# Performance work log

Measured on AMD Instinct MI355X. Metric: run time of the kernel, lower is better.

Reference implementation:

```python
import jax, jax.numpy as jnp
import numpy as np

IMSIZE = 128; R = 2; B = 2; C = 3; D = 64; Q = 128; M = 8; ITERS = 32
N = IMSIZE * IMSIZE
EPS = 1e-8


def _build_edges(S, r):
    # local (2r+1)^2 pixel neighborhood, as in build_perception(imsize, perception_size)
    ys, xs = np.meshgrid(np.arange(S), np.arange(S), indexing='ij')
    rows, cols = [], []
    for dy in range(-r, r + 1):
        for dx in range(-r, r + 1):
            ny, nx = ys + dy, xs + dx
            ok = (ny >= 0) & (ny < S) & (nx >= 0) & (nx < S)
            rows.append((ys * S + xs)[ok])
            cols.append((ny * S + nx)[ok])
    return (np.concatenate(rows).astype(np.int32), np.concatenate(cols).astype(np.int32))


def _conv(x, w, b=None):
    y = jax.lax.conv_general_dilated(x, w, (1, 1), 'SAME', dimension_numbers=('NHWC', 'HWIO', 'NHWC'))
    return y if b is None else y + b


def _bn(x, g, b):
    mu = x.mean((0, 1, 2))
    var = x.var((0, 1, 2))
    return (x - mu) * jax.lax.rsqrt(var + 1e-5) * g + b


def _resblock(f, w1, g1, t1, w2, g2, t2):
    h = jax.nn.relu(_bn(_conv(f, w1), g1, t1))
    h = _bn(_conv(h, w2), g2, t2)
    return jax.nn.relu(f + h)


def _forward(x, w_bb1, b_bb1, w_bb2, b_bb2,
             w_k1, g_k1, t_k1, w_k2, g_k2, t_k2, w_kp, b_kp,
             w_q1, g_q1, t_q1, w_q2, g_q2, t_q2, w_qp,
             h0, row, col, agent_idx):
    # conv backbone (preserves spatial resolution)
    f = jax.nn.relu(_conv(x, w_bb1, b_bb1))
    f = jax.nn.relu(_conv(f, w_bb2, b_bb2))
    # key / query heads: ResidualBlock + 1x1 conv
    ks = _conv(_resblock(f, w_k1, g_k1, t_k1, w_k2, g_k2, t_k2), w_kp, b_kp).reshape(B, N, D)
    qs = _conv(_resblock(f, w_q1, g_q1, t_q1, w_q2, g_q2, t_q2), w_qp).reshape(B, N, D)
    # edge-gather cosine similarity (torch.cosine_similarity with eps=1e-8)
    qe = qs[:, row]          # [B, E, D]
    ke = ks[:, col]          # [B, E, D]
    weights = (qe * ke).sum(-1) / (
        jnp.maximum(jnp.linalg.norm(qe, axis=-1), EPS) *
        jnp.maximum(jnp.linalg.norm(ke, axis=-1), EPS))   # [B, E]

    # 32-iteration sparse adjacency propagation: h <- normalize(A @ h)
    def step(h, _):
        msg = jnp.zeros_like(h).at[:, row, :].add(weights[:, :, None] * h[:, col, :])
        h = msg / jnp.maximum(jnp.linalg.norm(msg, axis=-1, keepdims=True), EPS)
        return h, None

    h, _ = jax.lax.scan(step, h0, None, length=ITERS)     # [B, N, Q]

    # competition routing: pixels compete for M agent slots via cosine affinity
    pix = h / jnp.maximum(jnp.linalg.norm(h, axis=-1, keepdims=True), EPS)
    ag = pix[:, agent_idx]                                # [B, M, Q]
    sim = jnp.einsum('bnq,bmq->bnm', pix, ag)
    masks = jax.nn.softmax(sim * 10.0, axis=-1)           # [B, N, M]
    return masks.reshape(B, IMSIZE, IMSIZE, M).transpose(0, 3, 1, 2)  # [B, M, W, H]


def setup_inputs() -> dict:
    key = jax.random.key(0)
    k = jax.random.split(key, 12)
    s = 0.05
    row, col = _build_edges(IMSIZE, R)
    agent_idx = np.linspace(0, N - 1, M).astype(np.int32)
    return dict(
        x=jax.random.normal(k[0], (B, IMSIZE, IMSIZE, C), jnp.float32),
        w_bb1=jax.random.normal(k[1], (3, 3, C, D), jnp.float32) * s, b_bb1=jnp.zeros((D,), jnp.float32),
        w_bb2=jax.random.normal(k[2], (3, 3, D, D), jnp.float32) * s, b_bb2=jnp.zeros((D,), jnp.float32),
        w_k1=jax.random.normal(k[3], (3, 3, D, D), jnp.float32) * s,
        g_k1=jnp.ones((D,), jnp.float32), t_k1=jnp.zeros((D,), jnp.float32),
        w_k2=jax.random.normal(k[4], (3, 3, D, D), jnp.float32) * s,
        g_k2=jnp.ones((D,), jnp.float32), t_k2=jnp.zeros((D,), jnp.float32),
        w_kp=jax.random.normal(k[5], (1, 1, D, D), jnp.float32) * s, b_kp=jnp.zeros((D,), jnp.float32),
        w_q1=jax.random.normal(k[6], (3, 3, D, D), jnp.float32) * s,
        g_q1=jnp.ones((D,), jnp.float32), t_q1=jnp.zeros((D,), jnp.float32),
        w_q2=jax.random.normal(k[7], (3, 3, D, D), jnp.float32) * s,
        g_q2=jnp.ones((D,), jnp.float32), t_q2=jnp.zeros((D,), jnp.float32),
        w_qp=jax.random.normal(k[8], (1, 1, D, D), jnp.float32) * s,
        h0=jax.random.normal(k[9], (B, N, Q), jnp.float32),
        row=jnp.asarray(row), col=jnp.asarray(col),
        agent_idx=jnp.asarray(agent_idx),
    )


def reference(x, w_bb1, b_bb1, w_bb2, b_bb2,
              w_k1, g_k1, t_k1, w_k2, g_k2, t_k2, w_kp, b_kp,
              w_q1, g_q1, t_q1, w_q2, g_q2, t_q2, w_qp,
              h0, row, col, agent_idx):
    return _forward(x, w_bb1, b_bb1, w_bb2, b_bb2,
                    w_k1, g_k1, t_k1, w_k2, g_k2, t_k2, w_kp, b_kp,
                    w_q1, g_q1, t_q1, w_q2, g_q2, t_q2, w_qp,
                    h0, row, col, agent_idx)
```

## Files before the change

### kernel.cpp

```cpp
#include <hip/hip_runtime.h>
#include <math.h>

#define NPIX 16384
#define EPSF 1e-8f

typedef float f32x4 __attribute__((ext_vector_type(4)));
typedef short s16x8 __attribute__((ext_vector_type(8)));

__device__ __forceinline__ float wred64(float s){
  s += __shfl_xor(s, 32); s += __shfl_xor(s, 16); s += __shfl_xor(s, 8);
  s += __shfl_xor(s, 4);  s += __shfl_xor(s, 2);  s += __shfl_xor(s, 1);
  return s;
}
__device__ __forceinline__ float rdlane(float v, int l){
  return __int_as_float(__builtin_amdgcn_readlane(__float_as_int(v), l));
}
__device__ __forceinline__ float dot4f(float4 a, float4 b, float acc){
  acc = fmaf(a.x,b.x,acc); acc = fmaf(a.y,b.y,acc);
  acc = fmaf(a.z,b.z,acc); acc = fmaf(a.w,b.w,acc);
  return acc;
}
__device__ __forceinline__ void bf16split(float v, unsigned short &hi, unsigned short &lo){
  unsigned u = __float_as_uint(v);
  unsigned r = u + 0x7FFFu + ((u >> 16) & 1u);
  hi = (unsigned short)(r >> 16);
  float hf = __uint_as_float(((unsigned)hi) << 16);
  float l = v - hf;
  unsigned u2 = __float_as_uint(l);
  unsigned r2 = u2 + 0x7FFFu + ((u2 >> 16) & 1u);
  lo = (unsigned short)(r2 >> 16);
}

__global__ __launch_bounds__(256) void prep_kernel(const float* __restrict__ w_bb2, const float* __restrict__ w_k1,
                            const float* __restrict__ w_k2, const float* __restrict__ w_q1,
                            const float* __restrict__ w_q2, const float* __restrict__ w_kp,
                            const float* __restrict__ w_qp, unsigned short* __restrict__ wh,
                            unsigned short* __restrict__ wl, float* __restrict__ wtp,
                            float* __restrict__ stats){
  int gid = blockIdx.x*256 + threadIdx.x;
  if (gid < 184320){
    int j = gid & 7;
    int t1 = gid >> 3;
    int lane = t1 & 63;
    int t2 = t1 >> 6;
    int kb = t2 % 18;
    int t3 = t2 / 18;
    int ct = t3 & 3;
    int c  = t3 >> 2;
    const float* src = c==0? w_bb2 : c==1? w_k1 : c==2? w_k2 : c==3? w_q1 : w_q2;
    int cout = ct*16 + (lane & 15);
    int k = kb*32 + (lane>>4)*8 + j;
    float v = src[k*64 + cout];
    unsigned short h,l; bf16split(v,h,l);
    wh[gid] = h; wl[gid] = l;
  } else if (gid < 192512){
    int t = gid - 184320; int which = t >> 12; int d = t & 4095;
    const float* src = which ? w_qp : w_kp;
    int k = d & 3, cout = (d>>2) & 63, cin4 = d >> 8;
    wtp[t] = src[(cin4*4 + k)*64 + cout];
  } else if (gid < 193024){
    stats[gid - 192512] = 0.f;
  }
}

__global__ __launch_bounds__(256) void conv1_kernel(const float* __restrict__ x, const float* __restrict__ w,
                                                    const float* __restrict__ bias, float* __restrict__ out){
  int wv = blockIdx.x*4 + (threadIdx.x >> 6);
  int c  = threadIdx.x & 63;
  int p0 = wv << 3;
  int ub = __builtin_amdgcn_readfirstlane(p0);
  int b  = ub >> 14; int i0 = ub & (NPIX-1);
  int y  = i0 >> 7, x0 = i0 & 127;
  float wv_[9][3];
  #pragma unroll
  for (int t=0;t<9;++t)
    #pragma unroll
    for (int ci=0;ci<3;++ci) wv_[t][ci] = w[(t*3+ci)*64 + c];
  float bv = bias[c];
  float acc[8];
  #pragma unroll
  for (int p=0;p<8;++p) acc[p] = bv;
  for (int ky=0; ky<3; ++ky){
    int ny = y + ky - 1;
    if ((unsigned)ny >= 128u) continue;
    const float* rowp = x + ((b<<14) + ny*128)*3;
    for (int kx=0; kx<3; ++kx){
      int t = ky*3 + kx;
      #pragma unroll
      for (int p=0;p<8;++p){
        int col = x0 + p + kx - 1;
        if ((unsigned)col < 128u){
          const float* ip = rowp + col*3;
          acc[p] = fmaf(ip[0], wv_[t][0], acc[p]);
          acc[p] = fmaf(ip[1], wv_[t][1], acc[p]);
          acc[p] = fmaf(ip[2], wv_[t][2], acc[p]);
        }
      }
    }
  }
  float* op = out + (p0 << 6) + c;
  #pragma unroll
  for (int p=0;p<8;++p) op[p*64] = fmaxf(acc[p], 0.f);
}

__global__ __launch_bounds__(512) void conv3m_kernel(const float* __restrict__ in,
    const unsigned short* __restrict__ wh, const unsigned short* __restrict__ wl,
    const float* __restrict__ bias, int relu,
    const float* __restrict__ bnst, const float* __restrict__ bng, const float* __restrict__ bnb,
    float* __restrict__ out, float* __restrict__ ost){
  __shared__ char smem[50688];
  unsigned short* lhi = (unsigned short*)smem;
  float* lout = (float*)smem;
  __shared__ float la[64], lb[64];
  __shared__ float ls1[64], ls2[64];
  int blk = blockIdx.x;
  int xh = blk & 1, y = (blk>>1) & 127, b = blk >> 8;
  int x0 = xh << 6;
  int tid = threadIdx.x;
  if (tid < 64){
    float a = 1.f, bo = 0.f;
    if (bnst){
      float mu  = bnst[tid] * (1.f/32768.f);
      float var = bnst[64+tid] * (1.f/32768.f) - mu*mu;
      a  = bng[tid] * rsqrtf(var + 1e-5f);
      bo = bnb[tid] - mu*a;
    }
    la[tid] = a; lb[tid] = bo;
    ls1[tid] = 0.f; ls2[tid] = 0.f;
  }
  __syncthreads();
  for (int s = tid; s < 3168; s += 512){
    int pr = s >> 4, cq = s & 15;
    int ky = pr / 66, px = pr - ky*66;
    int ny = y + ky - 1, gx = x0 - 1 + px;
    float v0=0.f, v1=0.f, v2=0.f, v3=0.f;
    if ((unsigned)ny < 128u && (unsigned)gx < 128u){
      const float* ip = in + (((b<<14) + ny*128 + gx)<<6) + (cq<<2);
      float4 t = *(const float4*)ip;
      int c0 = cq<<2;
      v0 = fmaxf(fmaf(t.x, la[c0],   lb[c0]),   0.f);
      v1 = fmaxf(fmaf(t.y, la[c0+1], lb[c0+1]), 0.f);
      v2 = fmaxf(fmaf(t.z, la[c0+2], lb[c0+2]), 0.f);
      v3 = fmaxf(fmaf(t.w, la[c0+3], lb[c0+3]), 0.f);
    }
    unsigned short h0,l0,h1,l1,h2,l2,h3,l3;
    bf16split(v0,h0,l0); bf16split(v1,h1,l1); bf16split(v2,h2,l2); bf16split(v3,h3,l3);
    int slot = (cq >> 1) ^ (pr & 7);
    int byte = pr*128 + (slot<<4) + ((cq & 1) << 3);
    *(uint2*)(smem + byte) = make_uint2((unsigned)h0 | ((unsigned)h1<<16),
                                        (unsigned)h2 | ((unsigned)h3<<16));
    *(uint2*)(smem + 25344 + byte) = make_uint2((unsigned)l0 | ((unsigned)l1<<16),
                                                (unsigned)l2 | ((unsigned)l3<<16));
  }
  __syncthreads();
  int lane = tid & 63, wid = tid >> 6;
  int pxsub = wid & 3, ch = wid >> 2;
  int col16 = lane & 15, kgrp = lane >> 4;
  f32x4 acc0 = {0.f,0.f,0.f,0.f}, acc1 = acc0, acl0 = acc0, acl1 = acc0;
  int abase = (ch*2*18)*512 + lane*8;
  #pragma unroll
  for (int kb=0; kb<18; ++kb){
    int tap = kb >> 1;
    int ky = (tap >= 6) ? 2 : (tap >= 3 ? 1 : 0);
    int kx = tap - ky*3;
    int pr = ky*66 + pxsub*16 + col16 + kx;
    int ci0 = ((kb & 1) << 5) + (kgrp << 3);
    int byte = pr*128 + ((((ci0 >> 3) ^ (pr & 7))) << 4);
    s16x8 Bh = *(const s16x8*)(smem + byte);
    s16x8 Bl = *(const s16x8*)(smem + 25344 + byte);
    int ao = abase + kb*512;
    s16x8 Ah0 = *(const s16x8*)(wh + ao);
    s16x8 Al0 = *(const s16x8*)(wl + ao);
    s16x8 Ah1 = *(const s16x8*)(wh + ao + 9216);
    s16x8 Al1 = *(const s16x8*)(wl + ao + 9216);
    acc0 = __builtin_amdgcn_mfma_f32_16x16x32_bf16(Ah0, Bh, acc0, 0, 0, 0);
    acl0 = __builtin_amdgcn_mfma_f32_16x16x32_bf16(Ah0, Bl, acl0, 0, 0, 0);
    acc1 = __builtin_amdgcn_mfma_f32_16x16x32_bf16(Ah1, Bh, acc1, 0, 0, 0);
    acl1 = __builtin_amdgcn_mfma_f32_16x16x32_bf16(Ah1, Bl, acl1, 0, 0, 0);
    acl0 = __builtin_amdgcn_mfma_f32_16x16x32_bf16(Al0, Bh, acl0, 0, 0, 0);
    acl1 = __builtin_amdgcn_mfma_f32_16x16x32_bf16(Al1, Bh, acl1, 0, 0, 0);
  }
  acc0 = acc0 + acl0;
  acc1 = acc1 + acl1;
  __syncthreads();
  int pxl = pxsub*16 + col16;
  int co0 = ch*32 + kgrp*4;
  *(f32x4*)(lout + pxl*68 + co0)      = acc0;
  *(f32x4*)(lout + pxl*68 + co0 + 16) = acc1;
  __syncthreads();
  {
    int px = tid >> 3, c8 = (tid & 7) << 3;
    const float* lp = lout + px*68 + c8;
    float r0[8];
    #pragma unroll
    for (int j=0;j<8;++j) r0[j] = lp[j];
    if (bias){
      #pragma unroll
      for (int j=0;j<8;++j) r0[j] += bias[c8+j];
    }
    if (relu){
      #pragma unroll
      for (int j=0;j<8;++j) r0[j] = fmaxf(r0[j], 0.f);
    }
    float* op = out + (((b<<14) + y*128 + x0 + px)<<6) + c8;
    #pragma unroll
    for (int j=0;j<8;++j) op[j] = r0[j];
    if (ost){
      float s1v[8], s2v[8];
      #pragma unroll
      for (int j=0;j<8;++j){ s1v[j] = r0[j]; s2v[j] = r0[j]*r0[j]; }
      #pragma unroll
      for (int m=8; m<64; m<<=1){
        #pragma unroll
        for (int j=0;j<8;++j){ s1v[j] += __shfl_xor(s1v[j], m); s2v[j] += __shfl_xor(s2v[j], m); }
      }
      int lane2 = tid & 63;
      if ((lane2 >> 3) == 0){
        int c0 = (lane2 & 7) << 3;
        #pragma unroll
        for (int j=0;j<8;++j){ atomicAdd(&ls1[c0+j], s1v[j]); atomicAdd(&ls2[c0+j], s2v[j]); }
      }
      __syncthreads();
      if (tid < 64){ atomicAdd(&ost[tid], ls1[tid]); atomicAdd(&ost[64+tid], ls2[tid]); }
    }
  }
}

__global__ __launch_bounds__(512) void conv3m2_kernel(const float* __restrict__ in,
    const unsigned short* __restrict__ whA, const unsigned short* __restrict__ wlA,
    const unsigned short* __restrict__ whB, const unsigned short* __restrict__ wlB,
    float* __restrict__ outA, float* __restrict__ ostA,
    float* __restrict__ outB, float* __restrict__ ostB){
  __shared__ char smem[50688];
  float* loutA = (float*)smem;
  float* loutB = (float*)smem + 4352;
  __shared__ float ls1A[64], ls2A[64], ls1B[64], ls2B[64];
  int blk = blockIdx.x;
  int xh = blk & 1, y = (blk>>1) & 127, b = blk >> 8;
  int x0 = xh << 6;
  int tid = threadIdx.x;
  if (tid < 64){ ls1A[tid]=0.f; ls2A[tid]=0.f; ls1B[tid]=0.f; ls2B[tid]=0.f; }
  __syncthreads();
  for (int s = tid; s < 3168; s += 512){
    int pr = s >> 4, cq = s & 15;
    int ky = pr / 66, px = pr - ky*66;
    int ny = y + ky - 1, gx = x0 - 1 + px;
    float v0=0.f, v1=0.f, v2=0.f, v3=0.f;
    if ((unsigned)ny < 128u && (unsigned)gx < 128u){
      const float* ip = in + (((b<<14) + ny*128 + gx)<<6) + (cq<<2);
      float4 t = *(const float4*)ip;
      v0 = t.x; v1 = t.y; v2 = t.z; v3 = t.w;
    }
    unsigned short h0,l0,h1,l1,h2,l2,h3,l3;
    bf16split(v0,h0,l0); bf16split(v1,h1,l1); bf16split(v2,h2,l2); bf16split(v3,h3,l3);
    int slot = (cq >> 1) ^ (pr & 7);
    int byte = pr*128 + (slot<<4) + ((cq & 1) << 3);
    *(uint2*)(smem + byte) = make_uint2((unsigned)h0 | ((unsigned)h1<<16),
                                        (unsigned)h2 | ((unsigned)h3<<16));
    *(uint2*)(smem + 25344 + byte) = make_uint2((unsigned)l0 | ((unsigned)l1<<16),
                                                (unsigned)l2 | ((unsigned)l3<<16));
  }
  __syncthreads();
  int lane = tid & 63, wid = tid >> 6;
  int pxsub = wid & 3, ch = wid >> 2;
  int col16 = lane & 15, kgrp = lane >> 4;
  f32x4 z = {0.f,0.f,0.f,0.f};
  f32x4 aA0=z, aA1=z, lA0=z, lA1=z, aB0=z, aB1=z, lB0=z, lB1=z;
  int abase = (ch*2*18)*512 + lane*8;
  #pragma unroll
  for (int kb=0; kb<18; ++kb){
    int tap = kb >> 1;
    int ky = (tap >= 6) ? 2 : (tap >= 3 ? 1 : 0);
    int kx = tap - ky*3;
    int pr = ky*66 + pxsub*16 + col16 + kx;
    int ci0 = ((kb & 1) << 5) + (kgrp << 3);
    int byte = pr*128 + ((((ci0 >> 3) ^ (pr & 7))) << 4);
    s16x8 Bh = *(const s16x8*)(smem + byte);
    s16x8 Bl = *(const s16x8*)(smem + 25344 + byte);
    int ao = abase + kb*512;
    s16x8 AhA0 = *(const s16x8*)(whA + ao);
    s16x8 AlA0 = *(const s16x8*)(wlA + ao);
    s16x8 AhA1 = *(const s16x8*)(whA + ao + 9216);
    s16x8 AlA1 = *(const s16x8*)(wlA + ao + 9216);
    s16x8 AhB0 = *(const s16x8*)(whB + ao);
    s16x8 AlB0 = *(const s16x8*)(wlB + ao);
    s16x8 AhB1 = *(const s16x8*)(whB + ao + 9216);
    s16x8 AlB1 = *(const s16x8*)(wlB + ao + 9216);
    aA0 = __builtin_amdgcn_mfma_f32_16x16x32_bf16(AhA0, Bh, aA0, 0, 0, 0);
    lA0 = __builtin_amdgcn_mfma_f32_16x16x32_bf16(AhA0, Bl, lA0, 0, 0, 0);
    aA1 = __builtin_amdgcn_mfma_f32_16x16x32_bf16(AhA1, Bh, aA1, 0, 0, 0);
    lA1 = __builtin_amdgcn_mfma_f32_16x16x32_bf16(AhA1, Bl, lA1, 0, 0, 0);
    lA0 = __builtin_amdgcn_mfma_f32_16x16x32_bf16(AlA0, Bh, lA0, 0, 0, 0);
    lA1 = __builtin_amdgcn_mfma_f32_16x16x32_bf16(AlA1, Bh, lA1, 0, 0, 0);
    aB0 = __builtin_amdgcn_mfma_f32_16x16x32_bf16(AhB0, Bh, aB0, 0, 0, 0);
    lB0 = __builtin_amdgcn_mfma_f32_16x16x32_bf16(AhB0, Bl, lB0, 0, 0, 0);
    aB1 = __builtin_amdgcn_mfma_f32_16x16x32_bf16(AhB1, Bh, aB1, 0, 0, 0);
    lB1 = __builtin_amdgcn_mfma_f32_16x16x32_bf16(AhB1, Bl, lB1, 0, 0, 0);
    lB0 = __builtin_amdgcn_mfma_f32_16x16x32_bf16(AlB0, Bh, lB0, 0, 0, 0);
    lB1 = __builtin_amdgcn_mfma_f32_16x16x32_bf16(AlB1, Bh, lB1, 0, 0, 0);
  }
  aA0 = aA0 + lA0; aA1 = aA1 + lA1;
  aB0 = aB0 + lB0; aB1 = aB1 + lB1;
  __syncthreads();
  int pxl = pxsub*16 + col16;
  int co0 = ch*32 + kgrp*4;
  *(f32x4*)(loutA + pxl*68 + co0)      = aA0;
  *(f32x4*)(loutA + pxl*68 + co0 + 16) = aA1;
  *(f32x4*)(loutB + pxl*68 + co0)      = aB0;
  *(f32x4*)(loutB + pxl*68 + co0 + 16) = aB1;
  __syncthreads();
  {
    int px = tid >> 3, c8 = (tid & 7) << 3;
    int lane2 = tid & 63;
    float rA[8], rB[8];
    #pragma unroll
    for (int j=0;j<8;++j){ rA[j] = loutA[px*68 + c8 + j]; rB[j] = loutB[px*68 + c8 + j]; }
    float* opA = outA + (((b<<14) + y*128 + x0 + px)<<6) + c8;
    float* opB = outB + (((b<<14) + y*128 + x0 + px)<<6) + c8;
    #pragma unroll
    for (int j=0;j<8;++j){ opA[j] = rA[j]; opB[j] = rB[j]; }
    float sA1[8], sA2[8], sB1[8], sB2[8];
    #pragma unroll
    for (int j=0;j<8;++j){ sA1[j]=rA[j]; sA2[j]=rA[j]*rA[j]; sB1[j]=rB[j]; sB2[j]=rB[j]*rB[j]; }
    #pragma unroll
    for (int m=8; m<64; m<<=1){
      #pragma unroll
      for (int j=0;j<8;++j){
        sA1[j] += __shfl_xor(sA1[j], m); sA2[j] += __shfl_xor(sA2[j], m);
        sB1[j] += __shfl_xor(sB1[j], m); sB2[j] += __shfl_xor(sB2[j], m);
      }
    }
    if ((lane2 >> 3) == 0){
      int c0 = (lane2 & 7) << 3;
      #pragma unroll
      for (int j=0;j<8;++j){
        atomicAdd(&ls1A[c0+j], sA1[j]); atomicAdd(&ls2A[c0+j], sA2[j]);
        atomicAdd(&ls1B[c0+j], sB1[j]); atomicAdd(&ls2B[c0+j], sB2[j]);
      }
    }
    __syncthreads();
    if (tid < 64){
      atomicAdd(&ostA[tid], ls1A[tid]); atomicAdd(&ostA[64+tid], ls2A[tid]);
      atomicAdd(&ostB[tid], ls1B[tid]); atomicAdd(&ostB[64+tid], ls2B[tid]);
    }
  }
}

__global__ __launch_bounds__(256) void resfuse2_kernel(float* __restrict__ tk, float* __restrict__ tq,
                                                       const float* __restrict__ f, const float* __restrict__ ST,
                                                       const float* __restrict__ gk, const float* __restrict__ bk,
                                                       const float* __restrict__ gq, const float* __restrict__ bq){
  int gid = blockIdx.x*256 + threadIdx.x;
  int isQ = gid >> 19;
  int idx4 = gid & 524287;
  float* t = isQ ? tq : tk;
  const float* stats = ST + (isQ ? 384 : 128);
  const float* g    = isQ ? gq : gk;
  const float* beta = isQ ? bq : bk;
  float4 v = ((float4*)t)[idx4];
  float4 fv = ((const float4*)f)[idx4];
  int c0 = (idx4 & 15) * 4;
  float a[4], bb[4];
  #pragma unroll
  for (int j=0;j<4;++j){
    int c = c0 + j;
    float mu  = stats[c]    * (1.f/32768.f);
    float var = stats[64+c] * (1.f/32768.f) - mu*mu;
    a[j]  = g[c] * rsqrtf(var + 1e-5f);
    bb[j] = beta[c] - mu*a[j];
  }
  v.x = fmaxf(fv.x + fmaf(v.x, a[0], bb[0]), 0.f);
  v.y = fmaxf(fv.y + fmaf(v.y, a[1], bb[1]), 0.f);
  v.z = fmaxf(fv.z + fmaf(v.z, a[2], bb[2]), 0.f);
  v.w = fmaxf(fv.w + fmaf(v.w, a[3], bb[3]), 0.f);
  ((float4*)t)[idx4] = v;
}

__global__ __launch_bounds__(256) void proj2_kernel(const float* __restrict__ rk, const float* __restrict__ rq,
                                                    const float* __restrict__ wtp, const float* __restrict__ bkp,
                                                    float* __restrict__ outk, float* __restrict__ outq,
                                                    float* __restrict__ nk, float* __restrict__ nq){
  int wvg = blockIdx.x*4 + (threadIdx.x >> 6);
  int isQ = wvg >> 12;
  int wv = wvg & 4095;
  int c  = threadIdx.x & 63;
  const float* r = isQ ? rq : rk;
  const float* wt1 = wtp + (isQ ? 4096 : 0);
  float* out = isQ ? outq : outk;
  float* nrm = isQ ? nq : nk;
  int p0 = wv << 3;
  int ub = __builtin_amdgcn_readfirstlane(p0);
  const float4* wq = (const float4*)wt1 + c;
  float4 w[16];
  #pragma unroll
  for (int q=0;q<16;++q) w[q] = wq[q*64];
  float bv = isQ ? 0.f : bkp[c];
  #pragma unroll
  for (int p=0;p<8;++p){
    const float* ip = r + ((ub + p) << 6);
    float a0 = bv, a1 = 0.f;
    #pragma unroll
    for (int q=0;q<16;q+=2){
      float4 i0 = *(const float4*)(ip + (q<<2));
      float4 i1 = *(const float4*)(ip + ((q+1)<<2));
      a0 = dot4f(i0, w[q],   a0);
      a1 = dot4f(i1, w[q+1], a1);
    }
    float acc = a0 + a1;
    out[((p0+p)<<6) + c] = acc;
    float s = wred64(acc*acc);
    if (c == 0) nrm[p0+p] = sqrtf(s);
  }
}

#define EW_PAD 68
__global__ __launch_bounds__(256) void edge_kernel(const float* __restrict__ qs, const float* __restrict__ ks,
                                                   const float* __restrict__ nq, const float* __restrict__ nk,
                                                   float* __restrict__ W){
  __shared__ float klds[100*EW_PAD];
  __shared__ float qlds[16*EW_PAD];
  int blk = blockIdx.x;
  int b = blk >> 10; int rem = blk & 1023;
  int y = rem >> 3; int x0 = (rem & 7) << 4;
  int tid = threadIdx.x;
  for (int s = tid; s < 1600; s += 256){
    int cin4 = s & 15; int col = (s >> 4) % 20; int r = (s >> 4) / 20;
    int ry = y - 2 + r; ry = ry < 0 ? 0 : (ry > 127 ? 127 : ry);
    int cx = x0 - 2 + col; cx = cx < 0 ? 0 : (cx > 127 ? 127 : cx);
    float4 v = *(const float4*)(ks + (((b<<14) + ry*128 + cx)<<6) + cin4*4);
    *(float4*)(klds + (r*20+col)*EW_PAD + cin4*4) = v;
  }
  {
    int cin4 = tid & 15; int px = tid >> 4;
    float4 v = *(const float4*)(qs + (((b<<14) + y*128 + x0 + px)<<6) + cin4*4);
    *(float4*)(qlds + px*EW_PAD + cin4*4) = v;
  }
  __syncthreads();
  #pragma unroll
  for (int pair=0; pair<2; ++pair){
    int t2 = tid + pair*256;
    int px = t2 >> 5; int o = t2 & 31;
    if (o < 25){
      int dy = o/5 - 2, dx = o%5 - 2;
      int yy = y + dy, xx = x0 + px + dx;
      bool valid = ((unsigned)yy < 128u) && ((unsigned)xx < 128u);
      const float* kq = klds + ((dy+2)*20 + (px+dx+2))*EW_PAD;
      const float* qq = qlds + px*EW_PAD;
      float a0 = 0.f, a1 = 0.f;
      #pragma unroll
      for (int q=0; q<16; q+=2){
        a0 = dot4f(*(const float4*)(qq + q*4),     *(const float4*)(kq + q*4),     a0);
        a1 = dot4f(*(const float4*)(qq + (q+1)*4), *(const float4*)(kq + (q+1)*4), a1);
      }
      float acc = a0 + a1;
      int gp = (b<<14) + y*128 + x0 + px;
      float wv_ = 0.f;
      if (valid){
        int gj = (b<<14) + yy*128 + xx;
        float rq = 1.f / fmaxf(nq[gp], EPSF);
        float rk = 1.f / fmaxf(nk[gj], EPSF);
        wv_ = acc * rq * rk;
      }
      W[gp*25 + o] = wv_;
    }
  }
}

__global__ __launch_bounds__(256) void mp_iter_kernel(const float* __restrict__ src, float* __restrict__ dst,
                                                      const float* __restrict__ W){
  int lane = threadIdx.x & 63;
  int wid  = threadIdx.x >> 6;
  int blk  = blockIdx.x;
  int xcd = blk & 7, s = blk >> 3;
  int row_id = xcd*32 + (s >> 3);
  int q8 = s & 7;
  int b = row_id >> 7, y = row_id & 127;
  int x0 = ((q8 << 2) + wid) << 2;
  int gp0 = (b << 14) + y*128 + x0;
  int lo = lane < 25 ? lane : 24;
  float wv[4];
  #pragma unroll
  for (int p=0;p<4;++p) wv[p] = W[(gp0+p)*25 + lo];
  const float* rp[5];
  #pragma unroll
  for (int r=0;r<5;++r){
    int ry = y - 2 + r; ry = ry < 0 ? 0 : (ry > 127 ? 127 : ry);
    rp[r] = src + (((b<<14) + ry*128) << 7) + lane;
  }
  float wa[5][5], wb[5][5];
  #pragma unroll
  for (int cc=0; cc<4; ++cc){
    int xc = x0 - 2 + cc; if (xc < 0) xc = 0;
    int off = xc << 7;
    #pragma unroll
    for (int r=0;r<5;++r){ wa[r][cc] = rp[r][off]; wb[r][cc] = rp[r][off + 64]; }
  }
  #pragma unroll
  for (int p=0;p<4;++p){
    int xl = x0 + p + 2; if (xl > 127) xl = 127;
    int off = xl << 7;
    #pragma unroll
    for (int r=0;r<5;++r){ wa[r][4] = rp[r][off]; wb[r][4] = rp[r][off + 64]; }
    float a0 = 0.f, a1 = 0.f;
    #pragma unroll
    for (int r=0;r<5;++r){
      #pragma unroll
      for (int cc=0;cc<5;++cc){
        float w = rdlane(wv[p], r*5+cc);
        a0 = fmaf(w, wa[r][cc], a0);
        a1 = fmaf(w, wb[r][cc], a1);
      }
    }
    float ss = wred64(a0*a0 + a1*a1);
    float sc = 1.f / fmaxf(sqrtf(ss), EPSF);
    float* dp = dst + ((gp0 + p) << 7) + lane;
    dp[0] = a0*sc; dp[64] = a1*sc;
    #pragma unroll
    for (int r=0;r<5;++r){
      #pragma unroll
      for (int cc=0;cc<4;++cc){ wa[r][cc] = wa[r][cc+1]; wb[r][cc] = wb[r][cc+1]; }
    }
  }
}

__global__ __launch_bounds__(256) void mp_last_kernel(const float* __restrict__ src, const float* __restrict__ W,
                                                      const int* __restrict__ agidx, float* __restrict__ out){
  int lane = threadIdx.x & 63;
  int wid  = threadIdx.x >> 6;
  int blk  = blockIdx.x;
  int xcd = blk & 7, s = blk >> 3;
  int row_id = xcd*32 + (s >> 2);
  int q4 = s & 3;
  int b = row_id >> 7, y = row_id & 127;
  int x0 = ((q4 << 2) + wid) << 3;
  int gp0 = (b << 14) + y*128 + x0;
  int lo = lane < 25 ? lane : 24;
  float av0[8], av1[8], isc[8];
  #pragma unroll
  for (int m=0;m<8;++m){
    int ai = agidx[m];
    int ay = ai >> 7, ax = ai & 127;
    float wva = W[((b<<14) + ai)*25 + lo];
    float aa0 = 0.f, aa1 = 0.f;
    #pragma unroll
    for (int r=0;r<5;++r){
      int ry = ay - 2 + r; ry = ry < 0 ? 0 : (ry > 127 ? 127 : ry);
      const float* rp = src + (((b<<14) + ry*128) << 7) + lane;
      #pragma unroll
      for (int cc=0;cc<5;++cc){
        int xc = ax - 2 + cc; xc = xc < 0 ? 0 : (xc > 127 ? 127 : xc);
        float w = rdlane(wva, r*5+cc);
        aa0 = fmaf(w, rp[xc<<7], aa0);
        aa1 = fmaf(w, rp[(xc<<7) + 64], aa1);
      }
    }
    float ssm = wred64(aa0*aa0 + aa1*aa1);
    isc[m] = 1.f / fmaxf(sqrtf(ssm), EPSF);
    av0[m] = aa0; av1[m] = aa1;
  }
  float wv[8];
  #pragma unroll
  for (int p=0;p<8;++p) wv[p] = W[(gp0+p)*25 + lo];
  const float* rp[5];
  #pragma unroll
  for (int r=0;r<5;++r){
    int ry = y - 2 + r; ry = ry < 0 ? 0 : (ry > 127 ? 127 : ry);
    rp[r] = src + (((b<<14) + ry*128) << 7) + lane;
  }
  float wa[5][5], wb[5][5];
  #pragma unroll
  for (int cc=0; cc<4; ++cc){
    int xc = x0 - 2 + cc; if (xc < 0) xc = 0;
    int off = xc << 7;
    #pragma unroll
    for (int r=0;r<5;++r){ wa[r][cc] = rp[r][off]; wb[r][cc] = rp[r][off + 64]; }
  }
  #pragma unroll
  for (int p=0;p<8;++p){
    int xl = x0 + p + 2; if (xl > 127) xl = 127;
    int off = xl << 7;
    #pragma unroll
    for (int r=0;r<5;++r){ wa[r][4] = rp[r][off]; wb[r][4] = rp[r][off + 64]; }
    float a0 = 0.f, a1 = 0.f;
    #pragma unroll
    for (int r=0;r<5;++r){
      #pragma unroll
      for (int cc=0;cc<5;++cc){
        float w = rdlane(wv[p], r*5+cc);
        a0 = fmaf(w, wa[r][cc], a0);
        a1 = fmaf(w, wb[r][cc], a1);
      }
    }
    float ss = wred64(a0*a0 + a1*a1);
    float sc = 1.f / fmaxf(sqrtf(ss), EPSF);
    float p0 = a0*sc, p1 = a1*sc;
    float sim[8];
    #pragma unroll
    for (int m=0;m<8;++m)
      sim[m] = wred64(p0*av0[m] + p1*av1[m]) * isc[m];
    float mx = sim[0];
    #pragma unroll
    for (int m=1;m<8;++m) mx = fmaxf(mx, sim[m]);
    float e[8]; float sum = 0.f;
    #pragma unroll
    for (int m=0;m<8;++m){ e[m] = __expf((sim[m]-mx)*10.f); sum += e[m]; }
    float rs = 1.f / sum;
    if (lane < 8){
      float val = e[0];
      #pragma unroll
      for (int m=1;m<8;++m) val = (lane==m) ? e[m] : val;
      out[(((b<<3)+lane)<<14) + y*128 + x0 + p] = val * rs;
    }
    #pragma unroll
    for (int r=0;r<5;++r){
      #pragma unroll
      for (int cc=0;cc<4;++cc){ wa[r][cc] = wa[r][cc+1]; wb[r][cc] = wb[r][cc+1]; }
    }
  }
}

extern "C" void kernel_launch(void* const* d_in, const int* in_sizes, int n_in,
                              void* d_out, int out_size, void* d_ws, size_t ws_size,
                              hipStream_t stream) {
  (void)in_sizes; (void)n_in; (void)out_size; (void)ws_size;
  const float* x     = (const float*)d_in[0];
  const float* w_bb1 = (const float*)d_in[1];
  const float* b_bb1 = (const float*)d_in[2];
  const float* w_bb2 = (const float*)d_in[3];
  const float* b_bb2 = (const float*)d_in[4];
  const float* w_k1  = (const float*)d_in[5];
  const float* g_k1  = (const float*)d_in[6];
  const float* t_k1  = (const float*)d_in[7];
  const float* w_k2  = (const float*)d_in[8];
  const float* g_k2  = (const float*)d_in[9];
  const float* t_k2  = (const float*)d_in[10];
  const float* w_kp  = (const float*)d_in[11];
  const float* b_kp  = (const float*)d_in[12];
  const float* w_q1  = (const float*)d_in[13];
  const float* g_q1  = (const float*)d_in[14];
  const float* t_q1  = (const float*)d_in[15];
  const float* w_q2  = (const float*)d_in[16];
  const float* g_q2  = (const float*)d_in[17];
  const float* t_q2  = (const float*)d_in[18];
  const float* w_qp  = (const float*)d_in[19];
  const float* h0    = (const float*)d_in[20];
  const int*   agidx = (const int*)d_in[23];
  float* out = (float*)d_out;
  float* ws  = (float*)d_ws;

  float* S0 = ws + 0;
  float* S1 = ws + 2097152;
  float* S2 = ws + 4194304;
  float* S3 = ws + 6291456;
  float* S4 = ws + 8388608;
  float* WW = ws + 12582912;
  float* NK = ws + 13402112;
  float* NQ = ws + 13434880;
  float* ST = ws + 13467648;
  float* WTp = ws + 13470208;
  unsigned short* WH = (unsigned short*)(ws + 13478400);
  unsigned short* WL = WH + 184320;
  float* HA = ws + 0;
  float* HB = ws + 4194304;

  prep_kernel<<<754, 256, 0, stream>>>(w_bb2, w_k1, w_k2, w_q1, w_q2, w_kp, w_qp, WH, WL, WTp, ST);
  conv1_kernel<<<1024, 256, 0, stream>>>(x, w_bb1, b_bb1, S0);
  conv3m_kernel<<<512, 512, 0, stream>>>(S0, WH + 0, WL + 0, b_bb2, 1, nullptr, nullptr, nullptr, S1, nullptr);
  conv3m2_kernel<<<512, 512, 0, stream>>>(S1, WH + 36864, WL + 36864, WH + 3*36864, WL + 3*36864,
                                          S2, ST + 0, S3, ST + 256);
  conv3m_kernel<<<512, 512, 0, stream>>>(S2, WH + 2*36864, WL + 2*36864, nullptr, 0, ST + 0, g_k1, t_k1, S0, ST + 128);
  conv3m_kernel<<<512, 512, 0, stream>>>(S3, WH + 4*36864, WL + 4*36864, nullptr, 0, ST + 256, g_q1, t_q1, S2, ST + 384);
  resfuse2_kernel<<<4096, 256, 0, stream>>>(S0, S2, S1, ST, g_k2, t_k2, g_q2, t_q2);
  proj2_kernel<<<2048, 256, 0, stream>>>(S0, S2, WTp, b_kp, S4, S3, NK, NQ);
  edge_kernel<<<2048, 256, 0, stream>>>(S3, S4, NQ, NK, WW);
  const float* sbuf = h0;
  for (int it = 0; it < 31; ++it){
    float* dbuf = (it & 1) ? HB : HA;
    mp_iter_kernel<<<2048, 256, 0, stream>>>(sbuf, dbuf, WW);
    sbuf = dbuf;
  }
  mp_last_kernel<<<1024, 256, 0, stream>>>(HA, WW, agidx, out);
}
```

Before: 612.2 us.

## Shrink conv tiles to 32 pixels and compute two rows per wave in propagation

```diff
diff --git a/kernel.cpp b/kernel.cpp
--- a/kernel.cpp
+++ b/kernel.cpp
@@ -103,19 +103,18 @@
   for (int p=0;p<8;++p) op[p*64] = fmaxf(acc[p], 0.f);
 }
 
-__global__ __launch_bounds__(512) void conv3m_kernel(const float* __restrict__ in,
+__global__ __launch_bounds__(256) void conv3m_kernel(const float* __restrict__ in,
     const unsigned short* __restrict__ wh, const unsigned short* __restrict__ wl,
     const float* __restrict__ bias, int relu,
     const float* __restrict__ bnst, const float* __restrict__ bng, const float* __restrict__ bnb,
     float* __restrict__ out, float* __restrict__ ost){
-  __shared__ char smem[50688];
-  unsigned short* lhi = (unsigned short*)smem;
+  __shared__ char smem[26112];
   float* lout = (float*)smem;
   __shared__ float la[64], lb[64];
   __shared__ float ls1[64], ls2[64];
   int blk = blockIdx.x;
-  int xh = blk & 1, y = (blk>>1) & 127, b = blk >> 8;
-  int x0 = xh << 6;
+  int xq = blk & 3, y = (blk>>2) & 127, b = blk >> 9;
+  int x0 = xq << 5;
   int tid = threadIdx.x;
   if (tid < 64){
     float a = 1.f, bo = 0.f;
@@ -129,9 +128,9 @@
     ls1[tid] = 0.f; ls2[tid] = 0.f;
   }
   __syncthreads();
-  for (int s = tid; s < 3168; s += 512){
+  for (int s = tid; s < 1632; s += 256){
     int pr = s >> 4, cq = s & 15;
-    int ky = pr / 66, px = pr - ky*66;
+    int ky = pr / 34, px = pr - ky*34;
     int ny = y + ky - 1, gx = x0 - 1 + px;
     float v0=0.f, v1=0.f, v2=0.f, v3=0.f;
     if ((unsigned)ny < 128u && (unsigned)gx < 128u){
@@ -149,12 +148,12 @@
     int byte = pr*128 + (slot<<4) + ((cq & 1) << 3);
     *(uint2*)(smem + byte) = make_uint2((unsigned)h0 | ((unsigned)h1<<16),
                                         (unsigned)h2 | ((unsigned)h3<<16));
-    *(uint2*)(smem + 25344 + byte) = make_uint2((unsigned)l0 | ((unsigned)l1<<16),
+    *(uint2*)(smem + 13056 + byte) = make_uint2((unsigned)l0 | ((unsigned)l1<<16),
                                                 (unsigned)l2 | ((unsigned)l3<<16));
   }
   __syncthreads();
   int lane = tid & 63, wid = tid >> 6;
-  int pxsub = wid & 3, ch = wid >> 2;
+  int pxsub = wid & 1, ch = wid >> 1;
   int col16 = lane & 15, kgrp = lane >> 4;
   f32x4 acc0 = {0.f,0.f,0.f,0.f}, acc1 = acc0, acl0 = acc0, acl1 = acc0;
   int abase = (ch*2*18)*512 + lane*8;
@@ -163,11 +162,11 @@
     int tap = kb >> 1;
     int ky = (tap >= 6) ? 2 : (tap >= 3 ? 1 : 0);
     int kx = tap - ky*3;
-    int pr = ky*66 + pxsub*16 + col16 + kx;
+    int pr = ky*34 + pxsub*16 + col16 + kx;
     int ci0 = ((kb & 1) << 5) + (kgrp << 3);
     int byte = pr*128 + ((((ci0 >> 3) ^ (pr & 7))) << 4);
     s16x8 Bh = *(const s16x8*)(smem + byte);
-    s16x8 Bl = *(const s16x8*)(smem + 25344 + byte);
+    s16x8 Bl = *(const s16x8*)(smem + 13056 + byte);
     int ao = abase + kb*512;
     s16x8 Ah0 = *(const s16x8*)(wh + ao);
     s16x8 Al0 = *(const s16x8*)(wl + ao);
@@ -226,24 +225,24 @@
   }
 }
 
-__global__ __launch_bounds__(512) void conv3m2_kernel(const float* __restrict__ in,
+__global__ __launch_bounds__(256) void conv3m2_kernel(const float* __restrict__ in,
     const unsigned short* __restrict__ whA, const unsigned short* __restrict__ wlA,
     const unsigned short* __restrict__ whB, const unsigned short* __restrict__ wlB,
     float* __restrict__ outA, float* __restrict__ ostA,
     float* __restrict__ outB, float* __restrict__ ostB){
-  __shared__ char smem[50688];
+  __shared__ char smem[26112];
   float* loutA = (float*)smem;
-  float* loutB = (float*)smem + 4352;
+  float* loutB = (float*)smem + 2176;
   __shared__ float ls1A[64], ls2A[64], ls1B[64], ls2B[64];
   int blk = blockIdx.x;
-  int xh = blk & 1, y = (blk>>1) & 127, b = blk >> 8;
-  int x0 = xh << 6;
+  int xq = blk & 3, y = (blk>>2) & 127, b = blk >> 9;
+  int x0 = xq << 5;
   int tid = threadIdx.x;
   if (tid < 64){ ls1A[tid]=0.f; ls2A[tid]=0.f; ls1B[tid]=0.f; ls2B[tid]=0.f; }
   __syncthreads();
-  for (int s = tid; s < 3168; s += 512){
+  for (int s = tid; s < 1632; s += 256){
     int pr = s >> 4, cq = s & 15;
-    int ky = pr / 66, px = pr - ky*66;
+    int ky = pr / 34, px = pr - ky*34;
     int ny = y + ky - 1, gx = x0 - 1 + px;
     float v0=0.f, v1=0.f, v2=0.f, v3=0.f;
     if ((unsigned)ny < 128u && (unsigned)gx < 128u){
@@ -257,12 +256,12 @@
     int byte = pr*128 + (slot<<4) + ((cq & 1) << 3);
     *(uint2*)(smem + byte) = make_uint2((unsigned)h0 | ((unsigned)h1<<16),
                                         (unsigned)h2 | ((unsigned)h3<<16));
-    *(uint2*)(smem + 25344 + byte) = make_uint2((unsigned)l0 | ((unsigned)l1<<16),
+    *(uint2*)(smem + 13056 + byte) = make_uint2((unsigned)l0 | ((unsigned)l1<<16),
                                                 (unsigned)l2 | ((unsigned)l3<<16));
   }
   __syncthreads();
   int lane = tid & 63, wid = tid >> 6;
-  int pxsub = wid & 3, ch = wid >> 2;
+  int pxsub = wid & 1, ch = wid >> 1;
   int col16 = lane & 15, kgrp = lane >> 4;
   f32x4 z = {0.f,0.f,0.f,0.f};
   f32x4 aA0=z, aA1=z, lA0=z, lA1=z, aB0=z, aB1=z, lB0=z, lB1=z;
@@ -272,11 +271,11 @@
     int tap = kb >> 1;
     int ky = (tap >= 6) ? 2 : (tap >= 3 ? 1 : 0);
     int kx = tap - ky*3;
-    int pr = ky*66 + pxsub*16 + col16 + kx;
+    int pr = ky*34 + pxsub*16 + col16 + kx;
     int ci0 = ((kb & 1) << 5) + (kgrp << 3);
     int byte = pr*128 + ((((ci0 >> 3) ^ (pr & 7))) << 4);
     s16x8 Bh = *(const s16x8*)(smem + byte);
-    s16x8 Bl = *(const s16x8*)(smem + 25344 + byte);
+    s16x8 Bl = *(const s16x8*)(smem + 13056 + byte);
     int ao = abase + kb*512;
     s16x8 AhA0 = *(const s16x8*)(whA + ao);
     s16x8 AlA0 = *(const s16x8*)(wlA + ao);
@@ -472,51 +471,66 @@
   int wid  = threadIdx.x >> 6;
   int blk  = blockIdx.x;
   int xcd = blk & 7, s = blk >> 3;
-  int row_id = xcd*32 + (s >> 3);
-  int q8 = s & 7;
-  int b = row_id >> 7, y = row_id & 127;
-  int x0 = ((q8 << 2) + wid) << 2;
-  int gp0 = (b << 14) + y*128 + x0;
+  int row_g = xcd*4 + (s >> 5);
+  int colg = s & 31;
+  int row0 = row_g*8 + wid*2;
+  int b = row0 >> 7, y0 = row0 & 127;
+  int x0 = colg << 2;
+  int base = b << 14;
   int lo = lane < 25 ? lane : 24;
-  float wv[4];
-  #pragma unroll
-  for (int p=0;p<4;++p) wv[p] = W[(gp0+p)*25 + lo];
-  const float* rp[5];
-  #pragma unroll
-  for (int r=0;r<5;++r){
-    int ry = y - 2 + r; ry = ry < 0 ? 0 : (ry > 127 ? 127 : ry);
-    rp[r] = src + (((b<<14) + ry*128) << 7) + lane;
-  }
-  float wa[5][5], wb[5][5];
+  float wv0[4], wv1[4];
+  #pragma unroll
+  for (int p=0;p<4;++p){
+    wv0[p] = W[(base + y0*128 + x0 + p)*25 + lo];
+    wv1[p] = W[(base + (y0+1)*128 + x0 + p)*25 + lo];
+  }
+  const float* rp[6];
+  #pragma unroll
+  for (int r=0;r<6;++r){
+    int ry = y0 - 2 + r; ry = ry < 0 ? 0 : (ry > 127 ? 127 : ry);
+    rp[r] = src + ((base + ry*128) << 7) + lane;
+  }
+  float wa[6][5], wb[6][5];
   #pragma unroll
   for (int cc=0; cc<4; ++cc){
     int xc = x0 - 2 + cc; if (xc < 0) xc = 0;
     int off = xc << 7;
     #pragma unroll
-    for (int r=0;r<5;++r){ wa[r][cc] = rp[r][off]; wb[r][cc] = rp[r][off + 64]; }
+    for (int r=0;r<6;++r){ wa[r][cc] = rp[r][off]; wb[r][cc] = rp[r][off + 64]; }
   }
   #pragma unroll
   for (int p=0;p<4;++p){
     int xl = x0 + p + 2; if (xl > 127) xl = 127;
     int off = xl << 7;
     #pragma unroll
-    for (int r=0;r<5;++r){ wa[r][4] = rp[r][off]; wb[r][4] = rp[r][off + 64]; }
-    float a0 = 0.f, a1 = 0.f;
+    for (int r=0;r<6;++r){ wa[r][4] = rp[r][off]; wb[r][4] = rp[r][off + 64]; }
+    float a0 = 0.f, a1 = 0.f, c0 = 0.f, c1 = 0.f;
     #pragma unroll
     for (int r=0;r<5;++r){
       #pragma unroll
       for (int cc=0;cc<5;++cc){
-        float w = rdlane(wv[p], r*5+cc);
-        a0 = fmaf(w, wa[r][cc], a0);
-        a1 = fmaf(w, wb[r][cc], a1);
-      }
-    }
-    float ss = wred64(a0*a0 + a1*a1);
-    float sc = 1.f / fmaxf(sqrtf(ss), EPSF);
-    float* dp = dst + ((gp0 + p) << 7) + lane;
-    dp[0] = a0*sc; dp[64] = a1*sc;
-    #pragma unroll
-    for (int r=0;r<5;++r){
+        float w0 = rdlane(wv0[p], r*5+cc);
+        a0 = fmaf(w0, wa[r][cc], a0);
+        a1 = fmaf(w0, wb[r][cc], a1);
+        float w1 = rdlane(wv1[p], r*5+cc);
+        c0 = fmaf(w1, wa[r+1][cc], c0);
+        c1 = fmaf(w1, wb[r+1][cc], c1);
+      }
+    }
+    {
+      float ss = wred64(a0*a0 + a1*a1);
+      float sc = 1.f / fmaxf(sqrtf(ss), EPSF);
+      float* dp = dst + ((base + y0*128 + x0 + p) << 7) + lane;
+      dp[0] = a0*sc; dp[64] = a1*sc;
+    }
+    {
+      float ss = wred64(c0*c0 + c1*c1);
+      float sc = 1.f / fmaxf(sqrtf(ss), EPSF);
+      float* dp = dst + ((base + (y0+1)*128 + x0 + p) << 7) + lane;
+      dp[0] = c0*sc; dp[64] = c1*sc;
+    }
+    #pragma unroll
+    for (int r=0;r<6;++r){
       #pragma unroll
       for (int cc=0;cc<4;++cc){ wa[r][cc] = wa[r][cc+1]; wb[r][cc] = wb[r][cc+1]; }
     }
@@ -665,18 +679,18 @@
 
   prep_kernel<<<754, 256, 0, stream>>>(w_bb2, w_k1, w_k2, w_q1, w_q2, w_kp, w_qp, WH, WL, WTp, ST);
   conv1_kernel<<<1024, 256, 0, stream>>>(x, w_bb1, b_bb1, S0);
-  conv3m_kernel<<<512, 512, 0, stream>>>(S0, WH + 0, WL + 0, b_bb2, 1, nullptr, nullptr, nullptr, S1, nullptr);
-  conv3m2_kernel<<<512, 512, 0, stream>>>(S1, WH + 36864, WL + 36864, WH + 3*36864, WL + 3*36864,
-                                          S2, ST + 0, S3, ST + 256);
-  conv3m_kernel<<<512, 512, 0, stream>>>(S2, WH + 2*36864, WL + 2*36864, nullptr, 0, ST + 0, g_k1, t_k1, S0, ST + 128);
-  conv3m_kernel<<<512, 512, 0, stream>>>(S3, WH + 4*36864, WL + 4*36864, nullptr, 0, ST + 256, g_q1, t_q1, S2, ST + 384);
+  conv3m_kernel<<<1024, 256, 0, stream>>>(S0, WH + 0, WL + 0, b_bb2, 1, nullptr, nullptr, nullptr, S1, nullptr);
+  conv3m2_kernel<<<1024, 256, 0, stream>>>(S1, WH + 36864, WL + 36864, WH + 3*36864, WL + 3*36864,
+                                           S2, ST + 0, S3, ST + 256);
+  conv3m_kernel<<<1024, 256, 0, stream>>>(S2, WH + 2*36864, WL + 2*36864, nullptr, 0, ST + 0, g_k1, t_k1, S0, ST + 128);
+  conv3m_kernel<<<1024, 256, 0, stream>>>(S3, WH + 4*36864, WL + 4*36864, nullptr, 0, ST + 256, g_q1, t_q1, S2, ST + 384);
   resfuse2_kernel<<<4096, 256, 0, stream>>>(S0, S2, S1, ST, g_k2, t_k2, g_q2, t_q2);
   proj2_kernel<<<2048, 256, 0, stream>>>(S0, S2, WTp, b_kp, S4, S3, NK, NQ);
   edge_kernel<<<2048, 256, 0, stream>>>(S3, S4, NQ, NK, WW);
   const float* sbuf = h0;
   for (int it = 0; it < 31; ++it){
     float* dbuf = (it & 1) ? HB : HA;
-    mp_iter_kernel<<<2048, 256, 0, stream>>>(sbuf, dbuf, WW);
+    mp_iter_kernel<<<1024, 256, 0, stream>>>(sbuf, dbuf, WW);
     sbuf = dbuf;
   }
   mp_last_kernel<<<1024, 256, 0, stream>>>(HA, WW, agidx, out);
```

After: 647.9 us. 5.8% more time.
